# Performance work log

Hardware: AMD Instinct MI355X
Metric: run time of the kernel (lower is better)

Reference implementation:

```python
import jax, jax.numpy as jnp
import numpy as np

NUM_GROUPS = 32
EPS = 1e-6


def group_norm(x, gamma, beta):
    # x: [b, c, h, w]
    b, c, h, w = x.shape
    g = NUM_GROUPS
    xg = x.reshape(b, g, c // g, h, w)
    mean = xg.mean(axis=(2, 3, 4), keepdims=True)
    var = xg.var(axis=(2, 3, 4), keepdims=True)
    xn = ((xg - mean) * jax.lax.rsqrt(var + EPS)).reshape(b, c, h, w)
    return xn * gamma[None, :, None, None] + beta[None, :, None, None]


def conv1x1(x, w, b):
    # x: [b, c, h, w], w: [out_c, in_c], b: [out_c]
    return jnp.einsum('bchw,oc->bohw', x, w) + b[None, :, None, None]


def setup_inputs() -> dict:
    key = jax.random.key(0)
    ks = jax.random.split(key, 11)
    B, C, H, W = 4, 512, 64, 64
    s = 1.0 / np.sqrt(C)
    inp = {
        'x': jax.random.normal(ks[0], (B, C, H, W), dtype=jnp.float32),
        'gn_gamma': jnp.ones((C,), dtype=jnp.float32),
        'gn_beta': jnp.zeros((C,), dtype=jnp.float32),
        'wq': jax.random.normal(ks[1], (C, C), dtype=jnp.float32) * s,
        'bq': jax.random.normal(ks[2], (C,), dtype=jnp.float32) * 0.01,
        'wk': jax.random.normal(ks[3], (C, C), dtype=jnp.float32) * s,
        'bk': jax.random.normal(ks[4], (C,), dtype=jnp.float32) * 0.01,
        'wv': jax.random.normal(ks[5], (C, C), dtype=jnp.float32) * s,
        'bv': jax.random.normal(ks[6], (C,), dtype=jnp.float32) * 0.01,
        'wo': jax.random.normal(ks[7], (C, C), dtype=jnp.float32) * s,
        'bo': jax.random.normal(ks[8], (C,), dtype=jnp.float32) * 0.01,
    }
    return inp


def reference(x, gn_gamma, gn_beta, wq, bq, wk, bk, wv, bv, wo, bo):
    b, c, h, w = x.shape
    h_ = group_norm(x, gn_gamma, gn_beta)
    q = conv1x1(h_, wq, bq).reshape(b, c, h * w)  # [b, c, n]
    k = conv1x1(h_, wk, bk).reshape(b, c, h * w)
    v = conv1x1(h_, wv, bv).reshape(b, c, h * w)
    scale = jnp.asarray(c, x.dtype) ** -0.5
    # attn[b, i, j] = softmax_j(q_i . k_j * scale)
    attn = jax.nn.softmax(jnp.einsum('bci,bcj->bij', q, k) * scale, axis=-1)
    # A[b, c, i] = sum_j attn[b, i, j] * v[b, c, j]
    A = jnp.einsum('bij,bcj->bci', attn, v).reshape(b, c, h, w)
    A = conv1x1(A, wo, bo)
    # NOTE: the original module multiplies (not adds) the input by the attention output
    return x * A
```

## Files before the change

kernel.cpp:

```cpp
#include <hip/hip_runtime.h>
#include <hip/hip_bf16.h>
#include <stdint.h>

typedef __bf16 bf16x8 __attribute__((ext_vector_type(8)));
typedef __bf16 bf16x4 __attribute__((ext_vector_type(4)));
typedef float f32x4 __attribute__((ext_vector_type(4)));

__device__ __forceinline__ void gload_lds16(const __bf16* g, __bf16* l) {
  __builtin_amdgcn_global_load_lds(
      (const __attribute__((address_space(1))) void*)g,
      (__attribute__((address_space(3))) void*)l, 16, 0, 0);
}

__global__ __launch_bounds__(256) void cvt4_kernel(const float* __restrict__ s0,
                                                   const float* __restrict__ s1,
                                                   const float* __restrict__ s2,
                                                   const float* __restrict__ s3,
                                                   __bf16* __restrict__ dst) {
  int i = blockIdx.x * 256 + threadIdx.x;
  const float* srcs[4] = {s0, s1, s2, s3};
  int m = i >> 18;
  dst[i] = (__bf16)srcs[m][i & 262143];
}

__global__ __launch_bounds__(256) void biascat_kernel(const float* __restrict__ bq,
                                                      const float* __restrict__ bk,
                                                      float* __restrict__ bqk) {
  int i = blockIdx.x * 256 + threadIdx.x;
  bqk[i] = (i < 512) ? bq[i] : bk[i - 512];
}

__global__ __launch_bounds__(256) void gn1a_kernel(const float* __restrict__ x,
                                                   __bf16* __restrict__ xbf,
                                                   float2* __restrict__ part) {
  const int tid = threadIdx.x;
  const size_t base4 = ((size_t)blockIdx.x * 8192) >> 2;
  const float4* x4 = (const float4*)x;
  bf16x4* o4 = (bf16x4*)xbf;

  float s1 = 0.f, s2 = 0.f;
#pragma unroll
  for (int j = 0; j < 8; ++j) {
    float4 t = x4[base4 + tid + j * 256];
    s1 += t.x + t.y + t.z + t.w;
    s2 += t.x * t.x + t.y * t.y + t.z * t.z + t.w * t.w;
    bf16x4 o;
    o[0] = (__bf16)t.x; o[1] = (__bf16)t.y; o[2] = (__bf16)t.z; o[3] = (__bf16)t.w;
    o4[base4 + tid + j * 256] = o;
  }
#pragma unroll
  for (int off = 32; off; off >>= 1) {
    s1 += __shfl_xor(s1, off);
    s2 += __shfl_xor(s2, off);
  }
  __shared__ float r1[4], r2[4];
  if ((tid & 63) == 0) { r1[tid >> 6] = s1; r2[tid >> 6] = s2; }
  __syncthreads();
  if (tid == 0)
    part[blockIdx.x] = float2{r1[0] + r1[1] + r1[2] + r1[3],
                              r2[0] + r2[1] + r2[2] + r2[3]};
}

__global__ __launch_bounds__(512) void gn1b_kernel(const float2* __restrict__ part,
                                                   const float* __restrict__ gamma,
                                                   const float* __restrict__ beta,
                                                   float2* __restrict__ gmbt) {
  const int b = blockIdx.x;
  const int t = threadIdx.x;
  __shared__ float sm[32], si[32];
  if (t < 32) {
    float s1 = 0.f, s2 = 0.f;
#pragma unroll
    for (int j = 0; j < 8; ++j) {
      float2 p = part[(b * 32 + t) * 8 + j];
      s1 += p.x; s2 += p.y;
    }
    const float mean = s1 * (1.f / 65536.f);
    const float var = s2 * (1.f / 65536.f) - mean * mean;
    sm[t] = mean;
    si[t] = rsqrtf(var + 1e-6f);
  }
  __syncthreads();
  const int g = t >> 4;
  const float gm = gamma[t] * si[g];
  gmbt[b * 512 + t] = float2{gm, beta[t] - sm[g] * gm};
}

__global__ __launch_bounds__(256) void gn2_kernel(const __bf16* __restrict__ xbf,
                                                  const float2* __restrict__ gmbt,
                                                  __bf16* __restrict__ hnT) {
  const int b = blockIdx.z;
  const int c0 = blockIdx.y * 64;
  const int n0 = blockIdx.x * 64;
  const int t = threadIdx.x;
  __shared__ __bf16 tile[64][72];

  {
    const int row = t >> 2;
    const int col = (t & 3) * 16;
    const __bf16* src = xbf + ((size_t)(b * 512 + c0 + row)) * 4096 + n0 + col;
    bf16x8 u0 = *(const bf16x8*)src;
    bf16x8 u1 = *(const bf16x8*)(src + 8);
    *(bf16x8*)&tile[row][col] = u0;
    *(bf16x8*)&tile[row][col + 8] = u1;
  }
  __syncthreads();
  {
    const int nrow = t >> 2;
    const int cc = (t & 3) * 16;
    bf16x8 o0, o1;
#pragma unroll
    for (int j = 0; j < 16; ++j) {
      const int c = c0 + cc + j;
      float2 s = gmbt[b * 512 + c];
      float val = (float)tile[cc + j][nrow] * s.x + s.y;
      if (j < 8) o0[j] = (__bf16)val; else o1[j - 8] = (__bf16)val;
    }
    __bf16* dst = hnT + ((size_t)b * 4096 + n0 + nrow) * 512 + c0 + cc;
    *(bf16x8*)dst = o0;
    *(bf16x8*)(dst + 8) = o1;
  }
}

__global__ __launch_bounds__(512) void qkexp_kernel(
    const __bf16* __restrict__ q, const __bf16* __restrict__ k,
    __bf16* __restrict__ S, long long sQ, long long sS, float scale) {
  constexpr int BST = 72;
  __shared__ __bf16 sm[8 * 8192 + 8 * 16 * BST];
  __bf16* smB = sm + 4 * 8192;
  __bf16* smE = sm + 8 * 8192;

  const int gx = gridDim.x, gxy = gx * gridDim.y;
  const int nwg = gxy * gridDim.z;
  int bid = blockIdx.x + gx * blockIdx.y + gxy * blockIdx.z;
  bid = (bid & 7) * (nwg >> 3) + (bid >> 3);
  const int bz = bid / gxy;
  const int rem = bid - bz * gxy;
  const int by = rem / gx, bx = rem - by * gx;
  const int tm0 = by * 1024, tn0 = bx * 256;

  const int t = threadIdx.x;
  const int lane = t & 63, wid = t >> 6;
  const int wr = wid >> 2, wc = wid & 3;

  const int scol = ((t & 3) * 8) ^ (((t >> 3) & 3) * 8);
  const __bf16* gA0 = q + (size_t)bz * sQ + (size_t)(tm0 + (t >> 2)) * 1024 + scol;
  const __bf16* gA1 = gA0 + (size_t)128 * 1024;
  const __bf16* gB0 = k + (size_t)bz * sQ + (size_t)(tn0 + (t >> 2)) * 1024 + scol;
  const __bf16* gB1 = gB0 + (size_t)128 * 1024;
  __bf16* dA = sm + t * 8;
  __bf16* dB = smB + t * 8;

  auto stageA = [&](int sig) {
    const int st_ = sig >> 4, ks = sig & 15, sl = sig & 3;
    const size_t off = (size_t)(st_ * 256) * 1024 + ks * 32;
    gload_lds16(gA0 + off, dA + sl * 8192);
    gload_lds16(gA1 + off, dA + sl * 8192 + 4096);
  };
  auto stageB = [&](int sig) {
    const int ks = sig & 15, sl = sig & 3;
    gload_lds16(gB0 + ks * 32, dB + sl * 8192);
    gload_lds16(gB1 + ks * 32, dB + sl * 8192 + 4096);
  };

  const int lr = lane & 15;
  const int kb = ((lane >> 4) * 16) ^ ((lr & 6) << 3);
  const __bf16* rdA = sm + (((wr * 128 + lr) * 64 + kb) >> 1);
  const __bf16* rdB = smB + (((wc * 64 + lr) * 64 + kb) >> 1);

  f32x4 acc[8][4];
#pragma unroll
  for (int m = 0; m < 8; ++m)
#pragma unroll
    for (int n = 0; n < 4; ++n) acc[m][n] = f32x4{0.f, 0.f, 0.f, 0.f};
  bf16x8 av[8];

  auto rdAfr = [&](int sl) {
#pragma unroll
    for (int m = 0; m < 8; ++m)
      av[m] = *(const bf16x8*)(rdA + sl * 8192 + m * 512);
  };
  auto mmaPh = [&](int sl, int nh) {
    bf16x8 bv[2];
#pragma unroll
    for (int j = 0; j < 2; ++j)
      bv[j] = *(const bf16x8*)(rdB + sl * 8192 + (nh * 2 + j) * 512);
    __builtin_amdgcn_s_barrier();
    __builtin_amdgcn_s_setprio(1);
#pragma unroll
    for (int m = 0; m < 8; ++m)
#pragma unroll
      for (int j = 0; j < 2; ++j)
        acc[m][nh * 2 + j] = __builtin_amdgcn_mfma_f32_16x16x32_bf16(
            av[m], bv[j], acc[m][nh * 2 + j], 0, 0, 0);
    __builtin_amdgcn_s_setprio(0);
    __builtin_amdgcn_s_barrier();
  };

  __bf16* bnc = smE + wid * 16 * BST;
  const int q4 = (lane >> 4) * 4;
  auto epilogue = [&](int st) {
    const int row0 = tm0 + st * 256 + wr * 128;
    const int wn = tn0 + wc * 64;
#pragma unroll
    for (int m = 0; m < 8; ++m) {
#pragma unroll
      for (int n = 0; n < 4; ++n)
#pragma unroll
        for (int r = 0; r < 4; ++r) {
          float val = acc[m][n][r] * scale;
          val = exp2f(val * 1.44269504f);
          bnc[(q4 + r) * BST + n * 16 + lr] = (__bf16)val;
        }
      const int rr = lane >> 3, c8 = (lane & 7) * 8;
      bf16x8 v0 = *(const bf16x8*)&bnc[rr * BST + c8];
      bf16x8 v1 = *(const bf16x8*)&bnc[(rr + 8) * BST + c8];
      __bf16* op = S + (size_t)bz * sS +
                   (size_t)(row0 + m * 16 + rr) * 4096 + wn + c8;
      *(bf16x8*)op = v0;
      *(bf16x8*)(op + (size_t)8 * 4096) = v1;
    }
  };

  stageA(0); stageB(0); stageA(1); stageB(1); stageA(2); stageB(2);
  asm volatile("s_waitcnt vmcnt(8)" ::: "memory");
  __builtin_amdgcn_s_barrier();

#pragma unroll 1
  for (int s = 0; s < 64; ++s) {
    const int sl = s & 3;
    rdAfr(sl);
    if (s + 3 < 64) stageA(s + 3);
    mmaPh(sl, 0);
    if (s + 3 < 64) stageB(s + 3);
    if (s >= 61) {
      if (s == 61) asm volatile("s_waitcnt vmcnt(4)" ::: "memory");
      else if (s == 62) asm volatile("s_waitcnt vmcnt(0)" ::: "memory");
    } else if ((s & 15) <= 1 && s > 15) {
      asm volatile("s_waitcnt vmcnt(24)" ::: "memory");
    } else {
      asm volatile("s_waitcnt vmcnt(8)" ::: "memory");
    }
    mmaPh(sl, 1);
    if ((s & 15) == 15) {
      epilogue(s >> 4);
      if (s < 63) {
#pragma unroll
        for (int m = 0; m < 8; ++m)
#pragma unroll
          for (int n = 0; n < 4; ++n) acc[m][n] = f32x4{0.f, 0.f, 0.f, 0.f};
      }
    }
  }
}

template <int BIASMODE, int RSUM, int EPI, int KC>
__global__ __launch_bounds__(256) void gemm4w_kernel(
    const __bf16* __restrict__ A, int lda, long long sA,
    const __bf16* __restrict__ Bm, int ldb, long long sB,
    void* __restrict__ Out, int ldo, long long sO,
    const float* __restrict__ bias, const __bf16* __restrict__ xmul,
    long long sX, float scale) {
  constexpr int SLOT = 4096;
  constexpr int BST = 72;
  __shared__ __bf16 sm[8 * SLOT];
  __bf16* smB = sm + 4 * SLOT;

  const int gx = gridDim.x, gxy = gx * gridDim.y;
  const int nwg = gxy * gridDim.z;
  int bid = blockIdx.x + gx * blockIdx.y + gxy * blockIdx.z;
  bid = (bid & 7) * (nwg >> 3) + (bid >> 3);
  const int bz = bid / gxy;
  const int rem = bid - bz * gxy;
  const int by = rem / gx, bx = rem - by * gx;
  const int tm0 = by * 128, tn0 = bx * 128;

  const int t = threadIdx.x;
  const int lane = t & 63, wid = t >> 6;
  const int wr = wid >> 1, wc = wid & 1;

  const __bf16* Az = A + (size_t)bz * sA;
  const __bf16* Bz = Bm + (size_t)bz * sB;

  const int scol = ((t & 3) * 8) ^ (((t >> 3) & 3) * 8);
  const __bf16* gA0 = Az + (size_t)(tm0 + (t >> 2)) * lda + scol;
  const __bf16* gA1 = gA0 + (size_t)64 * lda;
  const __bf16* gB0 = Bz + (size_t)(tn0 + (t >> 2)) * ldb + scol;
  const __bf16* gB1 = gB0 + (size_t)64 * ldb;
  __bf16* dA = sm + t * 8;
  __bf16* dB = smB + t * 8;

  auto stage = [&](int ks) {
    const int sl = ks & 3;
    gload_lds16(gA0 + (size_t)ks * 32, dA + sl * SLOT);
    gload_lds16(gA1 + (size_t)ks * 32, dA + sl * SLOT + 2048);
    gload_lds16(gB0 + (size_t)ks * 32, dB + sl * SLOT);
    gload_lds16(gB1 + (size_t)ks * 32, dB + sl * SLOT + 2048);
  };

  const int lr = lane & 15;
  const int kb = ((lane >> 4) * 16) ^ ((lr & 6) << 3);
  const __bf16* rdA = sm + (((wr * 64 + lr) * 64 + kb) >> 1);
  const __bf16* rdB = smB + (((wc * 64 + lr) * 64 + kb) >> 1);

  f32x4 acc[4][4];
#pragma unroll
  for (int i = 0; i < 4; ++i)
#pragma unroll
    for (int j = 0; j < 4; ++j) acc[i][j] = f32x4{0.f, 0.f, 0.f, 0.f};
  f32x4 acc1[4];
#pragma unroll
  for (int i = 0; i < 4; ++i) acc1[i] = f32x4{0.f, 0.f, 0.f, 0.f};
  bf16x8 onesf;
#pragma unroll
  for (int e = 0; e < 8; ++e) onesf[e] = (__bf16)1.0f;

  bf16x8 av[4], bv[4];

  auto rdfr = [&](int sl) {
#pragma unroll
    for (int m = 0; m < 4; ++m) av[m] = *(const bf16x8*)(rdA + sl * SLOT + m * 512);
#pragma unroll
    for (int n = 0; n < 4; ++n) bv[n] = *(const bf16x8*)(rdB + sl * SLOT + n * 512);
  };
  auto mma16 = [&] {
    __builtin_amdgcn_s_barrier();
    __builtin_amdgcn_s_setprio(1);
#pragma unroll
    for (int m = 0; m < 4; ++m)
#pragma unroll
      for (int n = 0; n < 4; ++n)
        acc[m][n] = __builtin_amdgcn_mfma_f32_16x16x32_bf16(av[m], bv[n], acc[m][n], 0, 0, 0);
    if constexpr (RSUM) {
#pragma unroll
      for (int m = 0; m < 4; ++m)
        acc1[m] = __builtin_amdgcn_mfma_f32_16x16x32_bf16(av[m], onesf, acc1[m], 0, 0, 0);
    }
    __builtin_amdgcn_s_setprio(0);
  };

  constexpr int TOT = KC / 32;

  stage(0); stage(1); stage(2);
  asm volatile("s_waitcnt vmcnt(8)" ::: "memory");
  __builtin_amdgcn_s_barrier();

#pragma unroll 1
  for (int s = 0; s < TOT - 3; ++s) {
    rdfr(s & 3);
    stage(s + 3);
    mma16();
    asm volatile("s_waitcnt vmcnt(8)" ::: "memory");
    __builtin_amdgcn_s_barrier();
  }
  rdfr((TOT - 3) & 3); mma16();
  asm volatile("s_waitcnt vmcnt(4)" ::: "memory");
  __builtin_amdgcn_s_barrier();
  rdfr((TOT - 2) & 3); mma16();
  asm volatile("s_waitcnt vmcnt(0)" ::: "memory");
  __builtin_amdgcn_s_barrier();
  rdfr((TOT - 1) & 3); mma16();
  __builtin_amdgcn_s_barrier();

  const int q4 = (lane >> 4) * 4;
  const int row0 = tm0 + wr * 64;
  const int wn = tn0 + wc * 64;
  if constexpr (EPI == 0) {
    __bf16* bnc = sm + wid * 16 * BST;
#pragma unroll
    for (int m = 0; m < 4; ++m) {
      float ri[4];
      if constexpr (RSUM) {
#pragma unroll
        for (int r = 0; r < 4; ++r) ri[r] = 1.0f / acc1[m][r];
      }
#pragma unroll
      for (int n = 0; n < 4; ++n)
#pragma unroll
        for (int r = 0; r < 4; ++r) {
          float val = acc[m][n][r] * scale;
          if constexpr (BIASMODE == 1) val += bias[wn + n * 16 + lr];
          if constexpr (BIASMODE == 2) val += bias[row0 + m * 16 + q4 + r];
          if constexpr (RSUM) val *= ri[r];
          bnc[(q4 + r) * BST + n * 16 + lr] = (__bf16)val;
        }
      const int rr = lane >> 3, c8 = (lane & 7) * 8;
      bf16x8 v0 = *(const bf16x8*)&bnc[rr * BST + c8];
      bf16x8 v1 = *(const bf16x8*)&bnc[(rr + 8) * BST + c8];
      __bf16* op = (__bf16*)Out + (size_t)bz * sO +
                   (size_t)(row0 + m * 16 + rr) * ldo + wn + c8;
      *(bf16x8*)op = v0;
      *(bf16x8*)(op + (size_t)8 * ldo) = v1;
    }
  } else {
#pragma unroll
    for (int m = 0; m < 4; ++m) {
#pragma unroll
      for (int r = 0; r < 4; ++r) {
        const int row = row0 + m * 16 + q4 + r;
        float brow = (BIASMODE == 2) ? bias[row] : 0.f;
        const size_t base = (size_t)bz * sO + (size_t)row * ldo;
#pragma unroll
        for (int n = 0; n < 4; ++n) {
          const int col = wn + n * 16 + lr;
          float val = acc[m][n][r] * scale + brow;
          if constexpr (BIASMODE == 1) val += bias[col];
          ((float*)Out)[base + col] =
              (float)xmul[(size_t)bz * sX + (size_t)row * ldo + col] * val;
        }
      }
    }
  }
}

extern "C" void kernel_launch(void* const* d_in, const int* in_sizes, int n_in,
                              void* d_out, int out_size, void* d_ws, size_t ws_size,
                              hipStream_t stream) {
  const int C = 512, N = 4096;
  const float* x = (const float*)d_in[0];
  const float* gng = (const float*)d_in[1];
  const float* gnb = (const float*)d_in[2];
  const float* wq = (const float*)d_in[3];
  const float* bq = (const float*)d_in[4];
  const float* wk = (const float*)d_in[5];
  const float* bk = (const float*)d_in[6];
  const float* wv = (const float*)d_in[7];
  const float* bv = (const float*)d_in[8];
  const float* wo = (const float*)d_in[9];
  const float* bo = (const float*)d_in[10];

  char* ws = (char*)d_ws;
  const size_t MB = 1ull << 20;
  const long long NC = (long long)N * C;
  const long long NN = (long long)N * N;
  const long long NQK = (long long)N * 1024;
  const bool batched = ws_size >= 194 * MB + 32768;

  __bf16 *S, *qkT, *a2T, *v, *xbf, *wqB;
  char* misc;
  if (batched) {
    S   = (__bf16*)(ws);
    qkT = (__bf16*)(ws + 128 * MB);
    a2T = qkT;
    v   = (__bf16*)(ws + 160 * MB);
    xbf = (__bf16*)(ws + 176 * MB);
    wqB = (__bf16*)(ws + 192 * MB);
    misc = ws + 194 * MB;
  } else {
    S   = (__bf16*)(ws);
    qkT = (__bf16*)(ws + 32 * MB);
    a2T = (__bf16*)(ws + 64 * MB);
    v   = (__bf16*)(ws + 80 * MB);
    xbf = (__bf16*)(ws + 96 * MB);
    wqB = (__bf16*)(ws + 112 * MB);
    misc = ws + 114 * MB;
  }
  __bf16* hnT = (__bf16*)ws;
  __bf16* wvB = wqB + 2 * 262144;
  __bf16* woB = wvB + 262144;
  float* bqk   = (float*)misc;
  float2* gmbt = (float2*)(misc + 4096);
  float2* part = (float2*)(misc + 20480);

  const float scl = 0.044194173824159216f;

  cvt4_kernel<<<4096, 256, 0, stream>>>(wq, wk, wv, wo, wqB);
  biascat_kernel<<<4, 256, 0, stream>>>(bq, bk, bqk);
  gn1a_kernel<<<1024, 256, 0, stream>>>(x, xbf, part);
  gn1b_kernel<<<4, 512, 0, stream>>>(part, gng, gnb, gmbt);
  gn2_kernel<<<dim3(64, 8, 4), 256, 0, stream>>>(xbf, gmbt, hnT);

  gemm4w_kernel<1, 0, 0, 512><<<dim3(8, 32, 4), 256, 0, stream>>>(
      hnT, C, NC, wqB, C, 0, qkT, 1024, NQK, bqk, nullptr, 0, 1.f);
  gemm4w_kernel<2, 0, 0, 512><<<dim3(32, 4, 4), 256, 0, stream>>>(
      wvB, C, 0, hnT, C, NC, v, N, NC, bv, nullptr, 0, 1.f);

  if (batched) {
    qkexp_kernel<<<dim3(16, 4, 4), 512, 0, stream>>>(
        qkT, qkT + 512, S, NQK, NN, scl);
    gemm4w_kernel<0, 1, 0, 4096><<<dim3(4, 32, 4), 256, 0, stream>>>(
        S, N, NN, v, N, NC, a2T, C, NC, nullptr, nullptr, 0, 1.f);
  } else {
    for (int b = 0; b < 4; ++b) {
      qkexp_kernel<<<dim3(16, 4, 1), 512, 0, stream>>>(
          qkT + (size_t)b * NQK, qkT + (size_t)b * NQK + 512, S, 0, 0, scl);
      gemm4w_kernel<0, 1, 0, 4096><<<dim3(4, 32, 1), 256, 0, stream>>>(
          S, N, 0, v + (size_t)b * NC, N, 0, a2T + (size_t)b * NC, C, 0,
          nullptr, nullptr, 0, 1.f);
    }
  }

  gemm4w_kernel<2, 0, 2, 512><<<dim3(32, 4, 4), 256, 0, stream>>>(
      woB, C, 0, a2T, C, NC, d_out, N, NC, bo, xbf, NC, 1.f);
}
```

Baseline: 264.2 us.

## Replace QK-exp kernel with gemm4w variant loading B fragments directly to registers

Removes the dedicated large-tile qkexp kernel and instead runs the QK^T+exp stage through the generic 128x128 gemm4w kernel with a new exp epilogue template flag. Adds a DIRB mode in which the B operand is read straight from global memory into register fragments, double-buffered, instead of being staged through LDS. This halves that kernel's LDS footprint, which may raise occupancy, and the mode is also used for the Q/K projection GEMM. In exchange it uses smaller tiles (more blocks, less reuse of A/B per block) and uncoalesced per-lane global reads for B, which could raise memory traffic.

```diff
diff --git a/kernel.cpp b/kernel.cpp
--- a/kernel.cpp
+++ b/kernel.cpp
@@ -122,139 +122,7 @@
   }
 }
 
-__global__ __launch_bounds__(512) void qkexp_kernel(
-    const __bf16* __restrict__ q, const __bf16* __restrict__ k,
-    __bf16* __restrict__ S, long long sQ, long long sS, float scale) {
-  constexpr int BST = 72;
-  __shared__ __bf16 sm[8 * 8192 + 8 * 16 * BST];
-  __bf16* smB = sm + 4 * 8192;
-  __bf16* smE = sm + 8 * 8192;
-
-  const int gx = gridDim.x, gxy = gx * gridDim.y;
-  const int nwg = gxy * gridDim.z;
-  int bid = blockIdx.x + gx * blockIdx.y + gxy * blockIdx.z;
-  bid = (bid & 7) * (nwg >> 3) + (bid >> 3);
-  const int bz = bid / gxy;
-  const int rem = bid - bz * gxy;
-  const int by = rem / gx, bx = rem - by * gx;
-  const int tm0 = by * 1024, tn0 = bx * 256;
-
-  const int t = threadIdx.x;
-  const int lane = t & 63, wid = t >> 6;
-  const int wr = wid >> 2, wc = wid & 3;
-
-  const int scol = ((t & 3) * 8) ^ (((t >> 3) & 3) * 8);
-  const __bf16* gA0 = q + (size_t)bz * sQ + (size_t)(tm0 + (t >> 2)) * 1024 + scol;
-  const __bf16* gA1 = gA0 + (size_t)128 * 1024;
-  const __bf16* gB0 = k + (size_t)bz * sQ + (size_t)(tn0 + (t >> 2)) * 1024 + scol;
-  const __bf16* gB1 = gB0 + (size_t)128 * 1024;
-  __bf16* dA = sm + t * 8;
-  __bf16* dB = smB + t * 8;
-
-  auto stageA = [&](int sig) {
-    const int st_ = sig >> 4, ks = sig & 15, sl = sig & 3;
-    const size_t off = (size_t)(st_ * 256) * 1024 + ks * 32;
-    gload_lds16(gA0 + off, dA + sl * 8192);
-    gload_lds16(gA1 + off, dA + sl * 8192 + 4096);
-  };
-  auto stageB = [&](int sig) {
-    const int ks = sig & 15, sl = sig & 3;
-    gload_lds16(gB0 + ks * 32, dB + sl * 8192);
-    gload_lds16(gB1 + ks * 32, dB + sl * 8192 + 4096);
-  };
-
-  const int lr = lane & 15;
-  const int kb = ((lane >> 4) * 16) ^ ((lr & 6) << 3);
-  const __bf16* rdA = sm + (((wr * 128 + lr) * 64 + kb) >> 1);
-  const __bf16* rdB = smB + (((wc * 64 + lr) * 64 + kb) >> 1);
-
-  f32x4 acc[8][4];
-#pragma unroll
-  for (int m = 0; m < 8; ++m)
-#pragma unroll
-    for (int n = 0; n < 4; ++n) acc[m][n] = f32x4{0.f, 0.f, 0.f, 0.f};
-  bf16x8 av[8];
-
-  auto rdAfr = [&](int sl) {
-#pragma unroll
-    for (int m = 0; m < 8; ++m)
-      av[m] = *(const bf16x8*)(rdA + sl * 8192 + m * 512);
-  };
-  auto mmaPh = [&](int sl, int nh) {
-    bf16x8 bv[2];
-#pragma unroll
-    for (int j = 0; j < 2; ++j)
-      bv[j] = *(const bf16x8*)(rdB + sl * 8192 + (nh * 2 + j) * 512);
-    __builtin_amdgcn_s_barrier();
-    __builtin_amdgcn_s_setprio(1);
-#pragma unroll
-    for (int m = 0; m < 8; ++m)
-#pragma unroll
-      for (int j = 0; j < 2; ++j)
-        acc[m][nh * 2 + j] = __builtin_amdgcn_mfma_f32_16x16x32_bf16(
-            av[m], bv[j], acc[m][nh * 2 + j], 0, 0, 0);
-    __builtin_amdgcn_s_setprio(0);
-    __builtin_amdgcn_s_barrier();
-  };
-
-  __bf16* bnc = smE + wid * 16 * BST;
-  const int q4 = (lane >> 4) * 4;
-  auto epilogue = [&](int st) {
-    const int row0 = tm0 + st * 256 + wr * 128;
-    const int wn = tn0 + wc * 64;
-#pragma unroll
-    for (int m = 0; m < 8; ++m) {
-#pragma unroll
-      for (int n = 0; n < 4; ++n)
-#pragma unroll
-        for (int r = 0; r < 4; ++r) {
-          float val = acc[m][n][r] * scale;
-          val = exp2f(val * 1.44269504f);
-          bnc[(q4 + r) * BST + n * 16 + lr] = (__bf16)val;
-        }
-      const int rr = lane >> 3, c8 = (lane & 7) * 8;
-      bf16x8 v0 = *(const bf16x8*)&bnc[rr * BST + c8];
-      bf16x8 v1 = *(const bf16x8*)&bnc[(rr + 8) * BST + c8];
-      __bf16* op = S + (size_t)bz * sS +
-                   (size_t)(row0 + m * 16 + rr) * 4096 + wn + c8;
-      *(bf16x8*)op = v0;
-      *(bf16x8*)(op + (size_t)8 * 4096) = v1;
-    }
-  };
-
-  stageA(0); stageB(0); stageA(1); stageB(1); stageA(2); stageB(2);
-  asm volatile("s_waitcnt vmcnt(8)" ::: "memory");
-  __builtin_amdgcn_s_barrier();
-
-#pragma unroll 1
-  for (int s = 0; s < 64; ++s) {
-    const int sl = s & 3;
-    rdAfr(sl);
-    if (s + 3 < 64) stageA(s + 3);
-    mmaPh(sl, 0);
-    if (s + 3 < 64) stageB(s + 3);
-    if (s >= 61) {
-      if (s == 61) asm volatile("s_waitcnt vmcnt(4)" ::: "memory");
-      else if (s == 62) asm volatile("s_waitcnt vmcnt(0)" ::: "memory");
-    } else if ((s & 15) <= 1 && s > 15) {
-      asm volatile("s_waitcnt vmcnt(24)" ::: "memory");
-    } else {
-      asm volatile("s_waitcnt vmcnt(8)" ::: "memory");
-    }
-    mmaPh(sl, 1);
-    if ((s & 15) == 15) {
-      epilogue(s >> 4);
-      if (s < 63) {
-#pragma unroll
-        for (int m = 0; m < 8; ++m)
-#pragma unroll
-          for (int n = 0; n < 4; ++n) acc[m][n] = f32x4{0.f, 0.f, 0.f, 0.f};
-      }
-    }
-  }
-}
-
-template <int BIASMODE, int RSUM, int EPI, int KC>
+template <int BIASMODE, int RSUM, int EPI, int DIRB, int EEXP, int KC>
 __global__ __launch_bounds__(256) void gemm4w_kernel(
     const __bf16* __restrict__ A, int lda, long long sA,
     const __bf16* __restrict__ Bm, int ldb, long long sB,
@@ -263,8 +131,9 @@
     long long sX, float scale) {
   constexpr int SLOT = 4096;
   constexpr int BST = 72;
-  __shared__ __bf16 sm[8 * SLOT];
-  __bf16* smB = sm + 4 * SLOT;
+  constexpr int NSM = DIRB ? (4 * SLOT) : (8 * SLOT);
+  __shared__ __bf16 sm[NSM];
+  __bf16* smB = sm + (DIRB ? 0 : 4 * SLOT);
 
   const int gx = gridDim.x, gxy = gx * gridDim.y;
   const int nwg = gxy * gridDim.z;
@@ -290,15 +159,19 @@
   __bf16* dA = sm + t * 8;
   __bf16* dB = smB + t * 8;
 
-  auto stage = [&](int ks) {
+  auto stageA = [&](int ks) {
     const int sl = ks & 3;
     gload_lds16(gA0 + (size_t)ks * 32, dA + sl * SLOT);
     gload_lds16(gA1 + (size_t)ks * 32, dA + sl * SLOT + 2048);
+  };
+  auto stageB = [&](int ks) {
+    const int sl = ks & 3;
     gload_lds16(gB0 + (size_t)ks * 32, dB + sl * SLOT);
     gload_lds16(gB1 + (size_t)ks * 32, dB + sl * SLOT + 2048);
   };
 
   const int lr = lane & 15;
+  const int lk = (lane >> 4) * 8;
   const int kb = ((lane >> 4) * 16) ^ ((lr & 6) << 3);
   const __bf16* rdA = sm + (((wr * 64 + lr) * 64 + kb) >> 1);
   const __bf16* rdB = smB + (((wc * 64 + lr) * 64 + kb) >> 1);
@@ -315,52 +188,99 @@
 #pragma unroll
   for (int e = 0; e < 8; ++e) onesf[e] = (__bf16)1.0f;
 
-  bf16x8 av[4], bv[4];
-
-  auto rdfr = [&](int sl) {
-#pragma unroll
-    for (int m = 0; m < 4; ++m) av[m] = *(const bf16x8*)(rdA + sl * SLOT + m * 512);
-#pragma unroll
-    for (int n = 0; n < 4; ++n) bv[n] = *(const bf16x8*)(rdB + sl * SLOT + n * 512);
-  };
-  auto mma16 = [&] {
+  bf16x8 av[4];
+  constexpr int TOT = KC / 32;
+
+  if constexpr (DIRB) {
+    const __bf16* pb[4];
+#pragma unroll
+    for (int n = 0; n < 4; ++n)
+      pb[n] = Bz + (size_t)(tn0 + wc * 64 + n * 16 + lr) * ldb + lk;
+
+    bf16x8 vb[2][4];
+    stageA(0); stageA(1); stageA(2);
+#pragma unroll
+    for (int n = 0; n < 4; ++n) vb[0][n] = *(const bf16x8*)(pb[n]);
+#pragma unroll
+    for (int n = 0; n < 4; ++n) vb[1][n] = *(const bf16x8*)(pb[n] + 32);
+    asm volatile("s_waitcnt vmcnt(4)" ::: "memory");
     __builtin_amdgcn_s_barrier();
-    __builtin_amdgcn_s_setprio(1);
-#pragma unroll
-    for (int m = 0; m < 4; ++m)
-#pragma unroll
-      for (int n = 0; n < 4; ++n)
-        acc[m][n] = __builtin_amdgcn_mfma_f32_16x16x32_bf16(av[m], bv[n], acc[m][n], 0, 0, 0);
-    if constexpr (RSUM) {
+
+#pragma unroll
+    for (int s = 0; s < TOT; ++s) {
 #pragma unroll
       for (int m = 0; m < 4; ++m)
-        acc1[m] = __builtin_amdgcn_mfma_f32_16x16x32_bf16(av[m], onesf, acc1[m], 0, 0, 0);
-    }
-    __builtin_amdgcn_s_setprio(0);
-  };
-
-  constexpr int TOT = KC / 32;
-
-  stage(0); stage(1); stage(2);
-  asm volatile("s_waitcnt vmcnt(8)" ::: "memory");
-  __builtin_amdgcn_s_barrier();
-
-#pragma unroll 1
-  for (int s = 0; s < TOT - 3; ++s) {
-    rdfr(s & 3);
-    stage(s + 3);
-    mma16();
+        av[m] = *(const bf16x8*)(rdA + (s & 3) * SLOT + m * 512);
+      if (s + 3 < TOT) stageA(s + 3);
+      __builtin_amdgcn_s_barrier();
+      __builtin_amdgcn_s_setprio(1);
+#pragma unroll
+      for (int m = 0; m < 4; ++m)
+#pragma unroll
+        for (int n = 0; n < 4; ++n)
+          acc[m][n] = __builtin_amdgcn_mfma_f32_16x16x32_bf16(
+              av[m], vb[s & 1][n], acc[m][n], 0, 0, 0);
+      if constexpr (RSUM) {
+#pragma unroll
+        for (int m = 0; m < 4; ++m)
+          acc1[m] = __builtin_amdgcn_mfma_f32_16x16x32_bf16(av[m], onesf, acc1[m], 0, 0, 0);
+      }
+      __builtin_amdgcn_s_setprio(0);
+      if (s + 2 < TOT) {
+#pragma unroll
+        for (int n = 0; n < 4; ++n)
+          vb[s & 1][n] = *(const bf16x8*)(pb[n] + (size_t)(s + 2) * 32);
+      }
+      if (s <= TOT - 4)      asm volatile("s_waitcnt vmcnt(6)" ::: "memory");
+      else if (s == TOT - 3) asm volatile("s_waitcnt vmcnt(4)" ::: "memory");
+      else if (s == TOT - 2) asm volatile("s_waitcnt vmcnt(0)" ::: "memory");
+      __builtin_amdgcn_s_barrier();
+    }
+  } else {
+    bf16x8 bv[4];
+    auto rdfr = [&](int sl) {
+#pragma unroll
+      for (int m = 0; m < 4; ++m) av[m] = *(const bf16x8*)(rdA + sl * SLOT + m * 512);
+#pragma unroll
+      for (int n = 0; n < 4; ++n) bv[n] = *(const bf16x8*)(rdB + sl * SLOT + n * 512);
+    };
+    auto mma16 = [&] {
+      __builtin_amdgcn_s_barrier();
+      __builtin_amdgcn_s_setprio(1);
+#pragma unroll
+      for (int m = 0; m < 4; ++m)
+#pragma unroll
+        for (int n = 0; n < 4; ++n)
+          acc[m][n] = __builtin_amdgcn_mfma_f32_16x16x32_bf16(av[m], bv[n], acc[m][n], 0, 0, 0);
+      if constexpr (RSUM) {
+#pragma unroll
+        for (int m = 0; m < 4; ++m)
+          acc1[m] = __builtin_amdgcn_mfma_f32_16x16x32_bf16(av[m], onesf, acc1[m], 0, 0, 0);
+      }
+      __builtin_amdgcn_s_setprio(0);
+    };
+
+    stageA(0); stageB(0); stageA(1); stageB(1); stageA(2); stageB(2);
     asm volatile("s_waitcnt vmcnt(8)" ::: "memory");
     __builtin_amdgcn_s_barrier();
-  }
-  rdfr((TOT - 3) & 3); mma16();
-  asm volatile("s_waitcnt vmcnt(4)" ::: "memory");
-  __builtin_amdgcn_s_barrier();
-  rdfr((TOT - 2) & 3); mma16();
-  asm volatile("s_waitcnt vmcnt(0)" ::: "memory");
-  __builtin_amdgcn_s_barrier();
-  rdfr((TOT - 1) & 3); mma16();
-  __builtin_amdgcn_s_barrier();
+
+#pragma unroll 1
+    for (int s = 0; s < TOT - 3; ++s) {
+      rdfr(s & 3);
+      stageA(s + 3); stageB(s + 3);
+      mma16();
+      asm volatile("s_waitcnt vmcnt(8)" ::: "memory");
+      __builtin_amdgcn_s_barrier();
+    }
+    rdfr((TOT - 3) & 3); mma16();
+    asm volatile("s_waitcnt vmcnt(4)" ::: "memory");
+    __builtin_amdgcn_s_barrier();
+    rdfr((TOT - 2) & 3); mma16();
+    asm volatile("s_waitcnt vmcnt(0)" ::: "memory");
+    __builtin_amdgcn_s_barrier();
+    rdfr((TOT - 1) & 3); mma16();
+    __builtin_amdgcn_s_barrier();
+  }
 
   const int q4 = (lane >> 4) * 4;
   const int row0 = tm0 + wr * 64;
@@ -381,6 +301,7 @@
           float val = acc[m][n][r] * scale;
           if constexpr (BIASMODE == 1) val += bias[wn + n * 16 + lr];
           if constexpr (BIASMODE == 2) val += bias[row0 + m * 16 + q4 + r];
+          if constexpr (EEXP) val = exp2f(val * 1.44269504f);
           if constexpr (RSUM) val *= ri[r];
           bnc[(q4 + r) * BST + n * 16 + lr] = (__bf16)val;
         }
@@ -470,26 +391,27 @@
   gn1b_kernel<<<4, 512, 0, stream>>>(part, gng, gnb, gmbt);
   gn2_kernel<<<dim3(64, 8, 4), 256, 0, stream>>>(xbf, gmbt, hnT);
 
-  gemm4w_kernel<1, 0, 0, 512><<<dim3(8, 32, 4), 256, 0, stream>>>(
+  gemm4w_kernel<1, 0, 0, 1, 0, 512><<<dim3(8, 32, 4), 256, 0, stream>>>(
       hnT, C, NC, wqB, C, 0, qkT, 1024, NQK, bqk, nullptr, 0, 1.f);
-  gemm4w_kernel<2, 0, 0, 512><<<dim3(32, 4, 4), 256, 0, stream>>>(
+  gemm4w_kernel<2, 0, 0, 0, 0, 512><<<dim3(32, 4, 4), 256, 0, stream>>>(
       wvB, C, 0, hnT, C, NC, v, N, NC, bv, nullptr, 0, 1.f);
 
   if (batched) {
-    qkexp_kernel<<<dim3(16, 4, 4), 512, 0, stream>>>(
-        qkT, qkT + 512, S, NQK, NN, scl);
-    gemm4w_kernel<0, 1, 0, 4096><<<dim3(4, 32, 4), 256, 0, stream>>>(
+    gemm4w_kernel<0, 0, 0, 1, 1, 512><<<dim3(32, 32, 4), 256, 0, stream>>>(
+        qkT, 1024, NQK, qkT + 512, 1024, NQK, S, N, NN, nullptr, nullptr, 0, scl);
+    gemm4w_kernel<0, 1, 0, 0, 0, 4096><<<dim3(4, 32, 4), 256, 0, stream>>>(
         S, N, NN, v, N, NC, a2T, C, NC, nullptr, nullptr, 0, 1.f);
   } else {
     for (int b = 0; b < 4; ++b) {
-      qkexp_kernel<<<dim3(16, 4, 1), 512, 0, stream>>>(
-          qkT + (size_t)b * NQK, qkT + (size_t)b * NQK + 512, S, 0, 0, scl);
-      gemm4w_kernel<0, 1, 0, 4096><<<dim3(4, 32, 1), 256, 0, stream>>>(
+      gemm4w_kernel<0, 0, 0, 1, 1, 512><<<dim3(32, 32, 1), 256, 0, stream>>>(
+          qkT + (size_t)b * NQK, 1024, 0, qkT + (size_t)b * NQK + 512, 1024, 0,
+          S, N, 0, nullptr, nullptr, 0, scl);
+      gemm4w_kernel<0, 1, 0, 0, 0, 4096><<<dim3(4, 32, 1), 256, 0, stream>>>(
           S, N, 0, v + (size_t)b * NC, N, 0, a2T + (size_t)b * NC, C, 0,
           nullptr, nullptr, 0, 1.f);
     }
   }
 
-  gemm4w_kernel<2, 0, 2, 512><<<dim3(32, 4, 4), 256, 0, stream>>>(
+  gemm4w_kernel<2, 0, 2, 0, 0, 512><<<dim3(32, 4, 4), 256, 0, stream>>>(
       woB, C, 0, a2T, C, NC, d_out, N, NC, bo, xbf, NC, 1.f);
 }
```

Result: slower. 339.9 us (+28.7%).
